# Optimization experiments

Measured on AMD Instinct MI355X. Metric: run time of the kernel, lower is better.

Reference implementation:

```python
import math
import jax, jax.numpy as jnp
import numpy as np

MAX_N = 3; MAX_L = 3
CUTOFF = 5.0; TB_CUTOFF = 4.0; NBLOCKS = 3
N_NODES = 5000; N_EDGES = 60000; N_TRIP = 400000
NELEM = 89; DN = 128; DE = 128; UNITS = 128; DEG = MAX_N * MAX_L

# zeros of spherical bessel j_l, l = 0..2, first 3 roots each
J_ROOTS = np.array([
    [3.141592653589793, 6.283185307179586, 9.42477796076938],
    [4.493409457909064, 7.725251836937707, 10.904121659428899],
    [5.763459196894550, 9.095011330476355, 12.322940970566582],
])

def _jl(l, x, xp):
    s, c = xp.sin(x), xp.cos(x)
    if l == 0:
        return s / x
    if l == 1:
        return s / x**2 - c / x
    if l == 2:
        return (3.0 / x**3 - 1.0 / x) * s - 3.0 * c / x**2
    return (15.0 / x**4 - 6.0 / x**2) * s - (15.0 / x**3 - 1.0 / x) * c

SBF_FACTOR = math.sqrt(2.0 / CUTOFF**3)
SBF_NORM = np.stack([np.abs(_jl(l + 1, J_ROOTS[l], np)) for l in range(MAX_L)])  # [3,3]

def sbf_expand(r):  # [n] -> [n, MAX_L*MAX_N], l-major (matches torch cat over l)
    cols = []
    for l in range(MAX_L):
        x = r[:, None] * (J_ROOTS[l] / CUTOFF)[None, :]
        cols.append(_jl(l, x, jnp) * (SBF_FACTOR / SBF_NORM[l])[None, :])
    return jnp.concatenate(cols, axis=1)

Y00 = 0.28209479177387814  # 0.5*sqrt(1/pi)
Y10 = 0.4886025119029199   # sqrt(3/(4pi))
Y20 = 0.31539156525252005  # 0.25*sqrt(5/pi)

def shf_expand(cos_t):  # [n] -> [n, MAX_L]  real Y_l0(theta)
    return jnp.stack([jnp.full_like(cos_t, Y00), Y10 * cos_t, Y20 * (3.0 * cos_t**2 - 1.0)], axis=1)

def poly_cutoff(r, c):
    x = r / c
    return 1.0 - 6.0 * x**5 + 15.0 * x**4 - 10.0 * x**3

def gated_mlp(x, Ws, bs, gWs, gbs):
    h = x
    for W, b in zip(Ws, bs):
        h = jax.nn.silu(h @ W + b)
    g = x
    n = len(gWs)
    for i, (W, b) in enumerate(zip(gWs, gbs)):
        g = g @ W + b
        g = jax.nn.sigmoid(g) if i == n - 1 else jax.nn.silu(g)
    return h * g

def _forward(pos, node_type, src, dst, t_src, t_dst, emb_table, edge_emb_W, edge_emb_b,
             tb_atom_W, tb_atom_b, tb_bond_W, tb_bond_Wg,
             W0, b0, W1, b1, W2, b2, gW0, gb0, gW1, gb1, gW2, gb2, wt,
             fW0, fb0, fW1, fb1, fW2, fb2):
    n_nodes = pos.shape[0]; n_edges = src.shape[0]
    bond_vec = pos[dst] - pos[src]                              # [E,3]
    bond_dist = jnp.sqrt(jnp.sum(bond_vec**2, axis=1) + 1e-12)  # [E]
    rbf = sbf_expand(bond_dist)                                 # [E,9]
    # triplet (line-graph edge) geometry
    v1, v2 = bond_vec[t_src], bond_vec[t_dst]
    cos_t = jnp.sum(v1 * v2, axis=1) / (bond_dist[t_src] * bond_dist[t_dst])
    three_basis = sbf_expand(bond_dist[t_dst]) * jnp.repeat(shf_expand(cos_t), MAX_N, axis=1)  # [T,9]
    cut3 = poly_cutoff(bond_dist, TB_CUTOFF)
    tw = (cut3[t_src] * cut3[t_dst])[:, None]                   # [T,1]
    end_atom = dst[t_dst]                                       # [T]
    node_feat = emb_table[node_type]                            # [N,DN]
    edge_feat = jax.nn.silu(rbf @ edge_emb_W + edge_emb_b)      # [E,DE]
    for k in range(NBLOCKS):
        # --- three-body interaction ---
        atoms = jax.nn.sigmoid(node_feat @ tb_atom_W[k] + tb_atom_b[k])  # [N,9]
        basis = three_basis * atoms[end_atom] * tw                        # [T,9]
        nb = jax.ops.segment_sum(basis, t_src, num_segments=n_edges)      # [E,9]
        edge_feat = edge_feat + jax.nn.silu(nb @ tb_bond_W[k]) * jax.nn.sigmoid(nb @ tb_bond_Wg[k])
        # --- graph conv: edge update ---
        x = jnp.concatenate([node_feat[src], node_feat[dst], edge_feat], axis=1)  # [E,384]
        e_upd = gated_mlp(x, (W0[k, 0], W1[k, 0], W2[k, 0]), (b0[k, 0], b1[k, 0], b2[k, 0]),
                          (gW0[k, 0], gW1[k, 0], gW2[k, 0]), (gb0[k, 0], gb1[k, 0], gb2[k, 0])) * (rbf @ wt[k, 0])
        edge_feat = edge_feat + e_upd
        # --- graph conv: node update (sum messages at destination) ---
        x = jnp.concatenate([node_feat[src], node_feat[dst], edge_feat], axis=1)
        mess = gated_mlp(x, (W0[k, 1], W1[k, 1], W2[k, 1]), (b0[k, 1], b1[k, 1], b2[k, 1]),
                         (gW0[k, 1], gW1[k, 1], gW2[k, 1]), (gb0[k, 1], gb1[k, 1], gb2[k, 1])) * (rbf @ wt[k, 1])
        node_feat = node_feat + jax.ops.segment_sum(mess, dst, num_segments=n_nodes)
    # ReduceReadOut('mean') over nodes (single graph) + final MLP
    v = jnp.mean(node_feat, axis=0)
    h = jax.nn.silu(v @ fW0 + fb0)
    h = jax.nn.silu(h @ fW1 + fb1)
    return jnp.squeeze(h @ fW2 + fb2)

def setup_inputs() -> dict:
    key = jax.random.key(0)
    ks = iter(jax.random.split(key, 64))
    def nrm(shape, fan_in):
        return jax.random.normal(next(ks), shape, dtype=jnp.float32) / math.sqrt(float(fan_in))
    pos = jax.random.normal(next(ks), (N_NODES, 3), dtype=jnp.float32) * 1.5
    node_type = jax.random.randint(next(ks), (N_NODES,), 0, NELEM, dtype=jnp.int32)
    src = jax.random.randint(next(ks), (N_EDGES,), 0, N_NODES, dtype=jnp.int32)
    dst = (src + 1 + jax.random.randint(next(ks), (N_EDGES,), 0, N_NODES - 1, dtype=jnp.int32)) % N_NODES
    t_src = jax.random.randint(next(ks), (N_TRIP,), 0, N_EDGES, dtype=jnp.int32)
    t_dst = jax.random.randint(next(ks), (N_TRIP,), 0, N_EDGES, dtype=jnp.int32)
    DIN = 2 * DN + DE
    z = lambda *s: jnp.zeros(s, jnp.float32)
    return dict(
        pos=pos, node_type=node_type, src=src, dst=dst, t_src=t_src, t_dst=t_dst,
        emb_table=nrm((NELEM, DN), 1.0),
        edge_emb_W=nrm((DEG, DE), DEG), edge_emb_b=z(DE),
        tb_atom_W=nrm((NBLOCKS, DN, DEG), DN), tb_atom_b=z(NBLOCKS, DEG),
        tb_bond_W=nrm((NBLOCKS, DEG, DE), DEG), tb_bond_Wg=nrm((NBLOCKS, DEG, DE), DEG),
        W0=nrm((NBLOCKS, 2, DIN, UNITS), DIN), b0=z(NBLOCKS, 2, UNITS),
        W1=nrm((NBLOCKS, 2, UNITS, UNITS), UNITS), b1=z(NBLOCKS, 2, UNITS),
        W2=nrm((NBLOCKS, 2, UNITS, DE), UNITS), b2=z(NBLOCKS, 2, DE),
        gW0=nrm((NBLOCKS, 2, DIN, UNITS), DIN), gb0=z(NBLOCKS, 2, UNITS),
        gW1=nrm((NBLOCKS, 2, UNITS, UNITS), UNITS), gb1=z(NBLOCKS, 2, UNITS),
        gW2=nrm((NBLOCKS, 2, UNITS, DE), UNITS), gb2=z(NBLOCKS, 2, DE),
        wt=nrm((NBLOCKS, 2, DEG, DE), DEG),
        fW0=nrm((DN, UNITS), DN), fb0=z(UNITS),
        fW1=nrm((UNITS, UNITS), UNITS), fb1=z(UNITS),
        fW2=nrm((UNITS, 1), UNITS), fb2=z(1))

def reference(pos, node_type, src, dst, t_src, t_dst, emb_table, edge_emb_W, edge_emb_b,
              tb_atom_W, tb_atom_b, tb_bond_W, tb_bond_Wg,
              W0, b0, W1, b1, W2, b2, gW0, gb0, gW1, gb1, gW2, gb2, wt,
              fW0, fb0, fW1, fb1, fW2, fb2):
    return _forward(pos, node_type, src, dst, t_src, t_dst, emb_table, edge_emb_W, edge_emb_b,
                    tb_atom_W, tb_atom_b, tb_bond_W, tb_bond_Wg,
                    W0, b0, W1, b1, W2, b2, gW0, gb0, gW1, gb1, gW2, gb2, wt,
                    fW0, fb0, fW1, fb1, fW2, fb2)
```

## Files before the change

kernel.cpp:

```cpp
#include <hip/hip_runtime.h>
#include <stdint.h>

typedef __attribute__((ext_vector_type(8))) short bf16x8;
typedef __attribute__((ext_vector_type(4))) float f32x4;
typedef __attribute__((ext_vector_type(4))) uint32_t u32x4;

#define XSS 392
#define HSS 144
#define TE 32

__device__ __forceinline__ float sigm(float x) { return __fdividef(1.0f, 1.0f + __expf(-x)); }
__device__ __forceinline__ float silu(float x) { return __fdividef(x, 1.0f + __expf(-x)); }
__device__ __forceinline__ short f2bf(float f) {
  uint32_t u = __float_as_uint(f);
  u = (u + 0x7fffu + ((u >> 16) & 1u)) >> 16;
  return (short)u;
}
__device__ __forceinline__ uint32_t cvt2(float lo, float hi) {
  uint32_t d;
  asm("v_cvt_pk_bf16_f32 %0, %1, %2" : "=v"(d) : "v"(lo), "v"(hi));
  return d;
}
__device__ __forceinline__ short f2bf1(float f) { return (short)cvt2(f, f); }

__device__ __forceinline__ float jl_eval(int l, float x) {
  float s, c;
  sincosf(x, &s, &c);
  float ix = 1.0f / x, ix2 = ix * ix;
  if (l == 0) return s * ix;
  if (l == 1) return s * ix2 - c * ix;
  if (l == 2) return (3.0f * ix2 * ix - ix) * s - 3.0f * ix2 * c;
  return (15.0f * ix2 * ix2 - 6.0f * ix2) * s - (15.0f * ix2 * ix - ix) * c;
}

__global__ void setup1_kernel(const int* __restrict__ ntb, const float* __restrict__ emb,
                              float* __restrict__ nf, int N,
                              const float* __restrict__ pos, const int* __restrict__ src,
                              const int* __restrict__ dst, float* __restrict__ bvec,
                              float* __restrict__ bdist, float* __restrict__ rbf,
                              float* __restrict__ cut3, int E,
                              const int* __restrict__ t_src, int* __restrict__ cnt_e,
                              int* __restrict__ cnt_n, int T) {
  int i = blockIdx.x * 256 + threadIdx.x;
  if (i < N * 128) {
    int n = i >> 7, c = i & 127;
    nf[i] = emb[ntb[n] * 128 + c];
  }
  if (i < E) {
    int s = src[i], d = dst[i];
    float dx = pos[d * 3 + 0] - pos[s * 3 + 0];
    float dy = pos[d * 3 + 1] - pos[s * 3 + 1];
    float dz = pos[d * 3 + 2] - pos[s * 3 + 2];
    float r = sqrtf(dx * dx + dy * dy + dz * dz + 1e-12f);
    bvec[i * 3 + 0] = dx; bvec[i * 3 + 1] = dy; bvec[i * 3 + 2] = dz;
    bdist[i] = r;
    const float roots[3][3] = {
        {3.141592653589793f, 6.283185307179586f, 9.42477796076938f},
        {4.493409457909064f, 7.725251836937707f, 10.904121659428899f},
        {5.763459196894550f, 9.095011330476355f, 12.322940970566582f}};
#pragma unroll
    for (int l = 0; l < 3; ++l) {
#pragma unroll
      for (int n = 0; n < 3; ++n) {
        float root = roots[l][n];
        float x = r * (root * 0.2f);
        float norm = fabsf(jl_eval(l + 1, root));
        rbf[i * 9 + l * 3 + n] = jl_eval(l, x) * (0.12649110640673518f / norm);
      }
    }
    float xx = r * 0.25f;
    float x3 = xx * xx * xx;
    cut3[i] = 1.0f - 6.0f * x3 * xx * xx + 15.0f * x3 * xx - 10.0f * x3;
    atomicAdd(&cnt_n[d], 1);
  }
  if (i < T) atomicAdd(&cnt_e[t_src[i]], 1);
}

__device__ void scan_chunk(const int* __restrict__ in, int* __restrict__ incl,
                           int* __restrict__ bsum, int L, int b) {
  __shared__ int sm[256];
  int i = b * 256 + threadIdx.x;
  int v = i < L ? in[i] : 0;
  sm[threadIdx.x] = v;
  __syncthreads();
  for (int st = 1; st < 256; st <<= 1) {
    int t = threadIdx.x >= st ? sm[threadIdx.x - st] : 0;
    __syncthreads();
    sm[threadIdx.x] += t;
    __syncthreads();
  }
  if (i < L) incl[i] = sm[threadIdx.x];
  if (threadIdx.x == 255) bsum[b] = sm[255];
}

__global__ void setup2_kernel(const float* __restrict__ rbf, const float* __restrict__ eW,
                              const float* __restrict__ eB, float* __restrict__ ef, int E,
                              const int* __restrict__ cnt_e, int* __restrict__ incl_e,
                              int* __restrict__ bsum_e, int ebk,
                              const int* __restrict__ cnt_n, int* __restrict__ incl_n,
                              int* __restrict__ bsum_n, int nbk, int N,
                              const float* __restrict__ nf, const float* __restrict__ taW,
                              const float* __restrict__ taB, float* __restrict__ atoms) {
  int b = blockIdx.x;
  if (b < ebk) scan_chunk(cnt_e, incl_e, bsum_e, E, b);
  else if (b < ebk + nbk) scan_chunk(cnt_n, incl_n, bsum_n, N, b - ebk);
  int i = b * 256 + threadIdx.x;
  if (i < E * 128) {
    int e = i >> 7, c = i & 127;
    float acc = eB[c];
#pragma unroll
    for (int d = 0; d < 9; ++d) acc += rbf[e * 9 + d] * eW[d * 128 + c];
    ef[i] = silu(acc);
  }
  if (i < N * 9) {
    int n = i / 9, d = i - n * 9;
    float acc = taB[d];
    for (int c = 0; c < 128; ++c) acc += nf[n * 128 + c] * taW[c * 9 + d];
    atoms[i] = sigm(acc);
  }
}

__global__ void scan_top2_kernel(int* __restrict__ bsum_e, int ne, int* __restrict__ bsum_n,
                                 int nn) {
  __shared__ int sm[1024];
  int* bs = blockIdx.x == 0 ? bsum_e : bsum_n;
  int nb = blockIdx.x == 0 ? ne : nn;
  int tid = threadIdx.x;
  int orig = tid < nb ? bs[tid] : 0;
  sm[tid] = orig;
  __syncthreads();
  for (int st = 1; st < 1024; st <<= 1) {
    int t = tid >= st ? sm[tid - st] : 0;
    __syncthreads();
    sm[tid] += t;
    __syncthreads();
  }
  if (tid < nb) bs[tid] = sm[tid] - orig;
}

__global__ void fin2_kernel(const int* __restrict__ cnt_e, const int* __restrict__ incl_e,
                            const int* __restrict__ bsum_e, int ebk, int* __restrict__ off_e,
                            int* __restrict__ cur_e, int E, const int* __restrict__ cnt_n,
                            const int* __restrict__ incl_n, const int* __restrict__ bsum_n,
                            int* __restrict__ off_n, int* __restrict__ cur_n, int N) {
  int b = blockIdx.x;
  if (b < ebk) {
    int i = b * 256 + threadIdx.x;
    if (i < E) {
      int o = incl_e[i] - cnt_e[i] + bsum_e[b];
      off_e[i] = o; cur_e[i] = o;
    }
  } else {
    int bb = b - ebk;
    int i = bb * 256 + threadIdx.x;
    if (i < N) {
      int o = incl_n[i] - cnt_n[i] + bsum_n[bb];
      off_n[i] = o; cur_n[i] = o;
    }
  }
}

__global__ void build_kernel(const int* __restrict__ t_src, const int* __restrict__ t_dst,
                             const int* __restrict__ dst, const float* __restrict__ bvec,
                             const float* __restrict__ bdist, const float* __restrict__ rbf,
                             const float* __restrict__ cut3, int* __restrict__ cur_e,
                             float* __restrict__ stbp, int* __restrict__ sa, int T,
                             int* __restrict__ cur_n, int* __restrict__ invp, int E) {
  int t = blockIdx.x * 256 + threadIdx.x;
  if (t < T) {
    int i = t_src[t], j = t_dst[t];
    float ax = bvec[i * 3], ay = bvec[i * 3 + 1], az = bvec[i * 3 + 2];
    float bx = bvec[j * 3], by = bvec[j * 3 + 1], bz = bvec[j * 3 + 2];
    float ct = (ax * bx + ay * by + az * bz) / (bdist[i] * bdist[j]);
    float tw = cut3[i] * cut3[j];
    float sh[3];
    sh[0] = 0.28209479177387814f * tw;
    sh[1] = 0.4886025119029199f * ct * tw;
    sh[2] = 0.31539156525252005f * (3.0f * ct * ct - 1.0f) * tw;
    int pos = atomicAdd(&cur_e[i], 1);
#pragma unroll
    for (int l = 0; l < 3; ++l)
#pragma unroll
      for (int n = 0; n < 3; ++n)
        stbp[(size_t)pos * 9 + l * 3 + n] = rbf[j * 9 + l * 3 + n] * sh[l];
    sa[pos] = dst[j];
  }
  if (t < E) {
    int pos = atomicAdd(&cur_n[dst[t]], 1);
    invp[t] = pos;
  }
}

__device__ void pack_one(const float* __restrict__ Wf, short* __restrict__ Wp, int K, int rr) {
  int per = 8 * (K / 32) * 64;
  int u = rr / per, r2 = rr - u * per;
  int lane = r2 & 63, tile = r2 >> 6;
  int kt = tile % (K / 32), nt = tile / (K / 32);
  int n = nt * 16 + (lane & 15);
  int k0 = kt * 32 + (lane >> 4) * 8;
  const float* s = Wf + (size_t)u * K * 128;
  bf16x8 v;
#pragma unroll
  for (int e = 0; e < 8; ++e) v[e] = f2bf(s[(size_t)(k0 + e) * 128 + n]);
  *(bf16x8*)(Wp + (size_t)u * K * 128 + (size_t)tile * 512 + lane * 8) = v;
}

__device__ void pack_pad9(const float* __restrict__ s, short* __restrict__ dp9, int l2) {
  int lane = l2 & 63, tile = l2 >> 6;
  int n = tile * 16 + (lane & 15);
  int k0 = (lane >> 4) * 8;
  bf16x8 v;
#pragma unroll
  for (int e = 0; e < 8; ++e)
    v[e] = (k0 + e < 9) ? f2bf(s[(size_t)(k0 + e) * 128 + n]) : (short)0;
  *(bf16x8*)(dp9 + tile * 512 + lane * 8) = v;
}

__global__ void pack_all_kernel(const float* __restrict__ W0, const float* __restrict__ G0,
                                const float* __restrict__ W1, const float* __restrict__ G1,
                                const float* __restrict__ W2, const float* __restrict__ G2,
                                const float* __restrict__ tbW, const float* __restrict__ tbG,
                                const float* __restrict__ WT,
                                short* __restrict__ pW0, short* __restrict__ pG0,
                                short* __restrict__ pW1, short* __restrict__ pG1,
                                short* __restrict__ pW2, short* __restrict__ pG2,
                                short* __restrict__ ptbW, short* __restrict__ ptbG,
                                short* __restrict__ pWT) {
  int idx = blockIdx.x * 256 + threadIdx.x;
  const int t384 = 6 * 8 * 12 * 64, t128 = 6 * 8 * 4 * 64;
  if (idx < t384) { pack_one(W0, pW0, 384, idx); return; }
  if (idx < 2 * t384) { pack_one(G0, pG0, 384, idx - t384); return; }
  int j = idx - 2 * t384;
  if (j < t128) { pack_one(W1, pW1, 128, j); return; }
  if (j < 2 * t128) { pack_one(G1, pG1, 128, j - t128); return; }
  if (j < 3 * t128) { pack_one(W2, pW2, 128, j - 2 * t128); return; }
  if (j < 4 * t128) { pack_one(G2, pG2, 128, j - 3 * t128); return; }
  j -= 4 * t128;
  if (j < 3072) {
    int kb = j >> 10;
    int w2 = (j >> 9) & 1;
    int l2 = j & 511;
    const float* s = (w2 ? tbG : tbW) + (size_t)kb * 9 * 128;
    short* dp = (w2 ? ptbG : ptbW) + (size_t)kb * 4096;
    pack_pad9(s, dp, l2);
    return;
  }
  j -= 3072;
  if (j < 3072) {
    int u = j >> 9;
    pack_pad9(WT + (size_t)u * 9 * 128, pWT + (size_t)u * 4096, j & 511);
  }
}

__device__ __forceinline__ f32x4 mfma16(bf16x8 a, bf16x8 b, f32x4 c) {
  return __builtin_amdgcn_mfma_f32_16x16x32_bf16(a, b, c, 0, 0, 0);
}

__device__ __forceinline__ void store_hg(short* hsb, short* gsb, int wave, int lane,
                                         const f32x4 (&aW)[2], const f32x4 (&aG)[2]) {
  const int lrow = lane & 15, lk = lane >> 4;
  const int colx = (wave * 16 + lrow) ^ (lk << 4);
#pragma unroll
  for (int mt = 0; mt < 2; ++mt)
#pragma unroll
    for (int rg = 0; rg < 4; ++rg) {
      int row = mt * 16 + lk * 4 + rg;
      hsb[row * HSS + colx] = f2bf1(silu(aW[mt][rg]));
      gsb[row * HSS + colx] = f2bf1(silu(aG[mt][rg]));
    }
}

__device__ __forceinline__ void layer128w(const short* hin, const short* gin,
                                          const short* __restrict__ pW,
                                          const short* __restrict__ pG,
                                          const float* __restrict__ Bh,
                                          const float* __restrict__ Bg, int wave, int lane,
                                          f32x4 (&aW)[2], f32x4 (&aG)[2]) {
  const int lrow = lane & 15, lk = lane >> 4;
  const int s0 = (lrow >> 2) & 3;
  float bw = Bh[wave * 16 + lrow], bg = Bg[wave * 16 + lrow];
  aW[0] = {bw, bw, bw, bw}; aW[1] = aW[0];
  aG[0] = {bg, bg, bg, bg}; aG[1] = aG[0];
#pragma unroll
  for (int kt = 0; kt < 4; ++kt) {
    int aoff = (kt * 32 + lk * 8) ^ (s0 << 4);
    bf16x8 ah0 = *(const bf16x8*)(hin + (size_t)lrow * HSS + aoff);
    bf16x8 ah1 = *(const bf16x8*)(hin + (size_t)(16 + lrow) * HSS + aoff);
    bf16x8 ag0 = *(const bf16x8*)(gin + (size_t)lrow * HSS + aoff);
    bf16x8 ag1 = *(const bf16x8*)(gin + (size_t)(16 + lrow) * HSS + aoff);
    bf16x8 bw8 = *(const bf16x8*)(pW + (size_t)(wave * 4 + kt) * 512 + lane * 8);
    bf16x8 bg8 = *(const bf16x8*)(pG + (size_t)(wave * 4 + kt) * 512 + lane * 8);
    aW[0] = mfma16(ah0, bw8, aW[0]);
    aW[1] = mfma16(ah1, bw8, aW[1]);
    aG[0] = mfma16(ag0, bg8, aG[0]);
    aG[1] = mfma16(ag1, bg8, aG[1]);
  }
}

__device__ __forceinline__ void run_chain(
    const short* xsb, short* hsb, short* gsb,
    const short* __restrict__ pW0, const short* __restrict__ pG0,
    const short* __restrict__ pW1, const short* __restrict__ pG1,
    const short* __restrict__ pW2, const short* __restrict__ pG2,
    const float* __restrict__ B0, const float* __restrict__ Gb0,
    const float* __restrict__ B1, const float* __restrict__ Gb1,
    const float* __restrict__ B2, const float* __restrict__ Gb2,
    int wave, int lane, f32x4 (&aW)[2], f32x4 (&aG)[2]) {
  const int lrow = lane & 15, lk = lane >> 4;
  const int s0 = (lrow >> 2) & 3;
  {
    float bw = B0[wave * 16 + lrow], bg = Gb0[wave * 16 + lrow];
    aW[0] = {bw, bw, bw, bw}; aW[1] = aW[0];
    aG[0] = {bg, bg, bg, bg}; aG[1] = aG[0];
  }
#pragma unroll
  for (int kt = 0; kt < 12; ++kt) {
    int al = kt * 32 + lk * 8;
    int aoff = (al < 256) ? al : (256 + ((al - 256) ^ (s0 << 4)));
    bf16x8 a0 = *(const bf16x8*)(xsb + (size_t)lrow * XSS + aoff);
    bf16x8 a1 = *(const bf16x8*)(xsb + (size_t)(16 + lrow) * XSS + aoff);
    bf16x8 bw8 = *(const bf16x8*)(pW0 + (size_t)(wave * 12 + kt) * 512 + lane * 8);
    bf16x8 bg8 = *(const bf16x8*)(pG0 + (size_t)(wave * 12 + kt) * 512 + lane * 8);
    aW[0] = mfma16(a0, bw8, aW[0]);
    aW[1] = mfma16(a1, bw8, aW[1]);
    aG[0] = mfma16(a0, bg8, aG[0]);
    aG[1] = mfma16(a1, bg8, aG[1]);
  }
  store_hg(hsb, gsb, wave, lane, aW, aG);
  __syncthreads();
  layer128w(hsb, gsb, pW1, pG1, B1, Gb1, wave, lane, aW, aG);
  __syncthreads();
  store_hg(hsb, gsb, wave, lane, aW, aG);
  __syncthreads();
  layer128w(hsb, gsb, pW2, pG2, B2, Gb2, wave, lane, aW, aG);
}

__global__ __launch_bounds__(512, 6) void gmlp_fused(
    const float* __restrict__ nf, float* __restrict__ ef, const float* __restrict__ rbf,
    const int* __restrict__ src, const int* __restrict__ dst,
    const float* __restrict__ stbp, const int* __restrict__ sa,
    const int* __restrict__ off_e, const int* __restrict__ cnt_e,
    const float* __restrict__ atoms, const int* __restrict__ invp,
    const short* __restrict__ ptbW, const short* __restrict__ ptbG,
    const short* __restrict__ pW0a, const short* __restrict__ pG0a,
    const short* __restrict__ pW1a, const short* __restrict__ pG1a,
    const short* __restrict__ pW2a, const short* __restrict__ pG2a,
    const float* __restrict__ B0a, const float* __restrict__ Gb0a,
    const float* __restrict__ B1a, const float* __restrict__ Gb1a,
    const float* __restrict__ B2a, const float* __restrict__ Gb2a,
    const short* __restrict__ pWTa,
    const short* __restrict__ pW0b, const short* __restrict__ pG0b,
    const short* __restrict__ pW1b, const short* __restrict__ pG1b,
    const short* __restrict__ pW2b, const short* __restrict__ pG2b,
    const float* __restrict__ B0b, const float* __restrict__ Gb0b,
    const float* __restrict__ B1b, const float* __restrict__ Gb1b,
    const float* __restrict__ B2b, const float* __restrict__ Gb2b,
    const short* __restrict__ pWTb,
    float* __restrict__ mbuf, int E, int writeEf) {
  __shared__ __align__(16) short xs[32][XSS];
  __shared__ __align__(16) short hs[32 * HSS];
  __shared__ __align__(16) short gs[32 * HSS];
  __shared__ __align__(16) short nbl[32][40];
  __shared__ __align__(16) short rbl[32][40];
  __shared__ int invs[32];
  const int tid = threadIdx.x;
  const int e0 = blockIdx.x * TE;
  const int r = tid >> 4, q = tid & 15;
  int eg = e0 + r; if (eg >= E) eg = E - 1;

  {
    float acc = 0.f;
    if (q < 9) {
      int o = off_e[eg], c = cnt_e[eg];
      for (int pp = o; pp < o + c; ++pp)
        acc += stbp[(size_t)pp * 9 + q] * atoms[(size_t)sa[pp] * 9 + q];
    }
    nbl[r][q] = (q < 9) ? f2bf1(acc) : (short)0;
    nbl[r][q + 16] = 0;
  }
  {
    const float* sp0 = nf + (size_t)src[eg] * 128;
    const float* sp1 = nf + (size_t)dst[eg] * 128;
#pragma unroll
    for (int seg = 0; seg < 2; ++seg) {
      const float* sp = seg == 0 ? sp0 : sp1;
      float4 f0 = *(const float4*)(sp + q * 8);
      float4 f1 = *(const float4*)(sp + q * 8 + 4);
      u32x4 v = {cvt2(f0.x, f0.y), cvt2(f0.z, f0.w), cvt2(f1.x, f1.y), cvt2(f1.z, f1.w)};
      *(u32x4*)&xs[r][seg * 128 + q * 8] = v;
    }
    for (int idx = tid; idx < 32 * 32; idx += 512) {
      int rr = idx >> 5, d = idx & 31;
      int ee = e0 + rr; if (ee >= E) ee = E - 1;
      rbl[rr][d] = (d < 9) ? f2bf1(rbf[ee * 9 + d]) : (short)0;
    }
    if (tid < 32) {
      int ee = e0 + tid; if (ee >= E) ee = E - 1;
      invs[tid] = invp[ee];
    }
  }
  __syncthreads();

  const int wave = tid >> 6;
  const int lane = tid & 63;
  const int lrow = lane & 15, lk = lane >> 4;
  const int col = wave * 16 + lrow;
  f32x4 aW[2], aG[2];
  float efb[2][4];

  {
    bf16x8 ta0 = *(const bf16x8*)&nbl[lrow][lk * 8];
    bf16x8 ta1 = *(const bf16x8*)&nbl[16 + lrow][lk * 8];
    bf16x8 tbw = *(const bf16x8*)(ptbW + wave * 512 + lane * 8);
    bf16x8 tbg = *(const bf16x8*)(ptbG + wave * 512 + lane * 8);
    f32x4 z = {0.f, 0.f, 0.f, 0.f};
    f32x4 tW0 = mfma16(ta0, tbw, z), tW1 = mfma16(ta1, tbw, z);
    f32x4 tG0 = mfma16(ta0, tbg, z), tG1 = mfma16(ta1, tbg, z);
#pragma unroll
    for (int mt = 0; mt < 2; ++mt)
#pragma unroll
      for (int rg = 0; rg < 4; ++rg) {
        int row = mt * 16 + lk * 4 + rg;
        int ec = e0 + row; if (ec >= E) ec = E - 1;
        float tw = mt == 0 ? tW0[rg] : tW1[rg];
        float tg = mt == 0 ? tG0[rg] : tG1[rg];
        float base = ef[(size_t)ec * 128 + col] + silu(tw) * sigm(tg);
        efb[mt][rg] = base;
        xs[row][256 + (col ^ (lk << 4))] = f2bf1(base);
      }
  }
  __syncthreads();

  run_chain(&xs[0][0], hs, gs, pW0a, pG0a, pW1a, pG1a, pW2a, pG2a,
            B0a, Gb0a, B1a, Gb1a, B2a, Gb2a, wave, lane, aW, aG);
  {
    bf16x8 ra0 = *(const bf16x8*)&rbl[lrow][lk * 8];
    bf16x8 ra1 = *(const bf16x8*)&rbl[16 + lrow][lk * 8];
    bf16x8 wtb = *(const bf16x8*)(pWTa + wave * 512 + lane * 8);
    f32x4 z = {0.f, 0.f, 0.f, 0.f};
    f32x4 wv0 = mfma16(ra0, wtb, z), wv1 = mfma16(ra1, wtb, z);
    const int cs = 256 + (col ^ (lk << 4));
#pragma unroll
    for (int mt = 0; mt < 2; ++mt)
#pragma unroll
      for (int rg = 0; rg < 4; ++rg) {
        int row = mt * 16 + lk * 4 + rg;
        int e = e0 + row;
        float wv = mt == 0 ? wv0[rg] : wv1[rg];
        float v = silu(aW[mt][rg]) * sigm(aG[mt][rg]) * wv;
        float nv = efb[mt][rg] + v;
        if (e < E && writeEf) ef[(size_t)e * 128 + col] = nv;
        xs[row][cs] = f2bf1(nv);
      }
  }
  __syncthreads();

  run_chain(&xs[0][0], hs, gs, pW0b, pG0b, pW1b, pG1b, pW2b, pG2b,
            B0b, Gb0b, B1b, Gb1b, B2b, Gb2b, wave, lane, aW, aG);
  {
    bf16x8 ra0 = *(const bf16x8*)&rbl[lrow][lk * 8];
    bf16x8 ra1 = *(const bf16x8*)&rbl[16 + lrow][lk * 8];
    bf16x8 wtb = *(const bf16x8*)(pWTb + wave * 512 + lane * 8);
    f32x4 z = {0.f, 0.f, 0.f, 0.f};
    f32x4 wv0 = mfma16(ra0, wtb, z), wv1 = mfma16(ra1, wtb, z);
#pragma unroll
    for (int mt = 0; mt < 2; ++mt)
#pragma unroll
      for (int rg = 0; rg < 4; ++rg) {
        int row = mt * 16 + lk * 4 + rg;
        int e = e0 + row;
        float wv = mt == 0 ? wv0[rg] : wv1[rg];
        float v = silu(aW[mt][rg]) * sigm(aG[mt][rg]) * wv;
        if (e < E) mbuf[(size_t)invs[row] * 128 + col] = v;
      }
  }
}

__global__ void node_gather_kernel(float* __restrict__ nf, const float* __restrict__ mbuf,
                                   const int* __restrict__ off_n, const int* __restrict__ cnt_n,
                                   const float* __restrict__ taW, const float* __restrict__ taB,
                                   float* __restrict__ atoms, int N, int doAtoms) {
  __shared__ float sm[2][128];
  int half = threadIdx.x >> 7, c = threadIdx.x & 127;
  int n = blockIdx.x * 2 + half;
  float v = 0.f;
  if (n < N) {
    int o = off_n[n], cnt = cnt_n[n];
    float acc = 0.f;
    for (int p = 0; p < cnt; ++p) acc += mbuf[(size_t)(o + p) * 128 + c];
    v = nf[(size_t)n * 128 + c] + acc;
    nf[(size_t)n * 128 + c] = v;
  }
  if (doAtoms) {
    sm[half][c] = v;
    __syncthreads();
    if (n < N && c < 9) {
      float a = taB[c];
      for (int cc = 0; cc < 128; ++cc) a += sm[half][cc] * taW[cc * 9 + c];
      atoms[n * 9 + c] = sigm(a);
    }
  }
}

__global__ void mean_kernel(const float* __restrict__ nf, float* __restrict__ partial, int N) {
  __shared__ float sm[256];
  int n0 = blockIdx.x * 256;
  int col = threadIdx.x & 127, half = threadIdx.x >> 7;
  int nend = n0 + 256 < N ? n0 + 256 : N;
  float s = 0.f;
  for (int n = n0 + half; n < nend; n += 2) s += nf[n * 128 + col];
  sm[threadIdx.x] = s;
  __syncthreads();
  if (threadIdx.x < 128)
    partial[blockIdx.x * 128 + threadIdx.x] = sm[threadIdx.x] + sm[threadIdx.x + 128];
}

__global__ void final_kernel(const float* __restrict__ partial, int nchunks, float Nf,
                             const float* __restrict__ fW0, const float* __restrict__ fb0,
                             const float* __restrict__ fW1, const float* __restrict__ fb1,
                             const float* __restrict__ fW2, const float* __restrict__ fb2,
                             float* __restrict__ out) {
  __shared__ float v[128], h[128], red[128];
  int tid = threadIdx.x;
  float s = 0.f;
  for (int b = 0; b < nchunks; ++b) s += partial[b * 128 + tid];
  v[tid] = s / Nf;
  __syncthreads();
  float acc = fb0[tid];
  for (int c = 0; c < 128; ++c) acc += v[c] * fW0[c * 128 + tid];
  h[tid] = silu(acc);
  __syncthreads();
  acc = fb1[tid];
  for (int c = 0; c < 128; ++c) acc += h[c] * fW1[c * 128 + tid];
  __syncthreads();
  v[tid] = silu(acc);
  __syncthreads();
  red[tid] = v[tid] * fW2[tid];
  __syncthreads();
  for (int st = 64; st > 0; st >>= 1) {
    if (tid < st) red[tid] += red[tid + st];
    __syncthreads();
  }
  if (tid == 0) out[0] = red[0] + fb2[0];
}

extern "C" void kernel_launch(void* const* d_in, const int* in_sizes, int n_in,
                              void* d_out, int out_size, void* d_ws, size_t ws_size,
                              hipStream_t stream) {
  const float* pos = (const float*)d_in[0];
  const int* node_type = (const int*)d_in[1];
  const int* src = (const int*)d_in[2];
  const int* dst = (const int*)d_in[3];
  const int* t_src = (const int*)d_in[4];
  const int* t_dst = (const int*)d_in[5];
  const float* emb = (const float*)d_in[6];
  const float* eW = (const float*)d_in[7];
  const float* eB = (const float*)d_in[8];
  const float* taW = (const float*)d_in[9];
  const float* taB = (const float*)d_in[10];
  const float* tbW = (const float*)d_in[11];
  const float* tbG = (const float*)d_in[12];
  const float* W0 = (const float*)d_in[13]; const float* B0 = (const float*)d_in[14];
  const float* W1 = (const float*)d_in[15]; const float* B1 = (const float*)d_in[16];
  const float* W2 = (const float*)d_in[17]; const float* B2 = (const float*)d_in[18];
  const float* G0 = (const float*)d_in[19]; const float* Gb0 = (const float*)d_in[20];
  const float* G1 = (const float*)d_in[21]; const float* Gb1 = (const float*)d_in[22];
  const float* G2 = (const float*)d_in[23]; const float* Gb2 = (const float*)d_in[24];
  const float* WT = (const float*)d_in[25];
  const float* fW0 = (const float*)d_in[26]; const float* fb0 = (const float*)d_in[27];
  const float* fW1 = (const float*)d_in[28]; const float* fb1 = (const float*)d_in[29];
  const float* fW2 = (const float*)d_in[30]; const float* fb2 = (const float*)d_in[31];

  const int N = in_sizes[1];
  const int E = in_sizes[2];
  const int T = in_sizes[4];

  char* p = (char*)d_ws;
  auto alloc = [&](size_t bytes) -> char* {
    char* r = p;
    p += (bytes + 255) & ~(size_t)255;
    return r;
  };
  float* nf    = (float*)alloc((size_t)N * 128 * 4);
  float* ef    = (float*)alloc((size_t)E * 128 * 4);
  float* mbuf  = (float*)alloc((size_t)E * 128 * 4);
  float* rbf   = (float*)alloc((size_t)E * 9 * 4);
  float* bvec  = (float*)alloc((size_t)E * 3 * 4);
  float* bdist = (float*)alloc((size_t)E * 4);
  float* cut3  = (float*)alloc((size_t)E * 4);
  float* stbp  = (float*)alloc((size_t)T * 9 * 4);
  int*   sa    = (int*)alloc((size_t)T * 4);
  float* atoms = (float*)alloc((size_t)N * 9 * 4);
  float* part  = (float*)alloc((size_t)64 * 128 * 4);
  int* cnt_all = (int*)alloc((size_t)(E + N) * 4);
  int* cnt_e = cnt_all, *cnt_n = cnt_all + E;
  int* incl_e = (int*)alloc((size_t)E * 4);
  int* incl_n = (int*)alloc((size_t)N * 4);
  int* off_e  = (int*)alloc((size_t)E * 4);
  int* off_n  = (int*)alloc((size_t)N * 4);
  int* cur_e  = (int*)alloc((size_t)E * 4);
  int* cur_n  = (int*)alloc((size_t)N * 4);
  int* invp   = (int*)alloc((size_t)E * 4);
  int* bsum_e = (int*)alloc((size_t)1024 * 4);
  int* bsum_n = (int*)alloc((size_t)1024 * 4);
  short* pW0s = (short*)alloc((size_t)6 * 384 * 128 * 2);
  short* pG0s = (short*)alloc((size_t)6 * 384 * 128 * 2);
  short* pW1s = (short*)alloc((size_t)6 * 128 * 128 * 2);
  short* pG1s = (short*)alloc((size_t)6 * 128 * 128 * 2);
  short* pW2s = (short*)alloc((size_t)6 * 128 * 128 * 2);
  short* pG2s = (short*)alloc((size_t)6 * 128 * 128 * 2);
  short* ptbWs = (short*)alloc((size_t)3 * 4096 * 2);
  short* ptbGs = (short*)alloc((size_t)3 * 4096 * 2);
  short* pWTs  = (short*)alloc((size_t)6 * 4096 * 2);
  (void)ws_size; (void)n_in; (void)out_size;

  const int ebk = (E + 255) / 256, nbk = (N + 255) / 256;

  pack_all_kernel<<<504, 256, 0, stream>>>(W0, G0, W1, G1, W2, G2, tbW, tbG, WT,
                                           pW0s, pG0s, pW1s, pG1s, pW2s, pG2s,
                                           ptbWs, ptbGs, pWTs);
  hipMemsetAsync(cnt_all, 0, (size_t)(E + N) * 4, stream);
  {
    int g1 = N * 128; if (E > g1) g1 = E; if (T > g1) g1 = T;
    setup1_kernel<<<(g1 + 255) / 256, 256, 0, stream>>>(
        node_type, emb, nf, N, pos, src, dst, bvec, bdist, rbf, cut3, E, t_src, cnt_e, cnt_n, T);
  }
  {
    int g2 = E * 128; int g2b = (ebk + nbk) * 256; if (g2b > g2) g2 = g2b;
    if (N * 9 > g2) g2 = N * 9;
    setup2_kernel<<<(g2 + 255) / 256, 256, 0, stream>>>(
        rbf, eW, eB, ef, E, cnt_e, incl_e, bsum_e, ebk, cnt_n, incl_n, bsum_n, nbk, N,
        nf, taW, taB, atoms);
  }
  scan_top2_kernel<<<2, 1024, 0, stream>>>(bsum_e, ebk, bsum_n, nbk);
  fin2_kernel<<<ebk + nbk, 256, 0, stream>>>(cnt_e, incl_e, bsum_e, ebk, off_e, cur_e, E,
                                             cnt_n, incl_n, bsum_n, off_n, cur_n, N);
  {
    int g3 = T > E ? T : E;
    build_kernel<<<(g3 + 255) / 256, 256, 0, stream>>>(t_src, t_dst, dst, bvec, bdist, rbf,
                                                       cut3, cur_e, stbp, sa, T, cur_n, invp, E);
  }

  const int gblocks = (E + TE - 1) / TE;
  for (int k = 0; k < 3; ++k) {
    size_t u0 = (size_t)(k * 2 + 0), u1 = u0 + 1;
    gmlp_fused<<<gblocks, 512, 0, stream>>>(
        nf, ef, rbf, src, dst, stbp, sa, off_e, cnt_e, atoms, invp,
        ptbWs + (size_t)k * 4096, ptbGs + (size_t)k * 4096,
        pW0s + u0 * 384 * 128, pG0s + u0 * 384 * 128, pW1s + u0 * 128 * 128,
        pG1s + u0 * 128 * 128, pW2s + u0 * 128 * 128, pG2s + u0 * 128 * 128,
        B0 + u0 * 128, Gb0 + u0 * 128, B1 + u0 * 128, Gb1 + u0 * 128, B2 + u0 * 128,
        Gb2 + u0 * 128, pWTs + u0 * 4096,
        pW0s + u1 * 384 * 128, pG0s + u1 * 384 * 128, pW1s + u1 * 128 * 128,
        pG1s + u1 * 128 * 128, pW2s + u1 * 128 * 128, pG2s + u1 * 128 * 128,
        B0 + u1 * 128, Gb0 + u1 * 128, B1 + u1 * 128, Gb1 + u1 * 128, B2 + u1 * 128,
        Gb2 + u1 * 128, pWTs + u1 * 4096,
        mbuf, E, k < 2 ? 1 : 0);
    int nk = k < 2 ? k + 1 : 0;
    node_gather_kernel<<<(N + 1) / 2, 256, 0, stream>>>(
        nf, mbuf, off_n, cnt_n, taW + (size_t)nk * 128 * 9, taB + (size_t)nk * 9,
        atoms, N, k < 2 ? 1 : 0);
  }

  int nchunks = (N + 255) / 256;
  mean_kernel<<<nchunks, 256, 0, stream>>>(nf, part, N);
  final_kernel<<<1, 128, 0, stream>>>(part, nchunks, (float)N, fW0, fb0, fW1, fb1, fW2, fb2,
                                      (float*)d_out);
}
```

Baseline: 516.3 us.

## Store edge features, messages and triplet bases in bf16 and hoist weight MFMAs

Edge features, per-edge messages and the three-body basis buffers move from fp32 to bf16 storage, roughly halving their global memory traffic in the fused edge kernel and the node gather. The edge feature row is now loaded as one vector into the shared tile during prologue staging, replacing scattered scalar global reads. Both rbf-weight MFMAs are hoisted to the start of the kernel. This keeps the residual edge state in bf16 between blocks, which costs accuracy, and the hoisted results raise register pressure.

```diff
diff --git a/kernel.cpp b/kernel.cpp
--- a/kernel.cpp
+++ b/kernel.cpp
@@ -4,6 +4,7 @@
 typedef __attribute__((ext_vector_type(8))) short bf16x8;
 typedef __attribute__((ext_vector_type(4))) float f32x4;
 typedef __attribute__((ext_vector_type(4))) uint32_t u32x4;
+typedef unsigned short ushort;
 
 #define XSS 392
 #define HSS 144
@@ -16,6 +17,7 @@
   u = (u + 0x7fffu + ((u >> 16) & 1u)) >> 16;
   return (short)u;
 }
+__device__ __forceinline__ float bf2f(ushort u) { return __uint_as_float(((uint32_t)u) << 16); }
 __device__ __forceinline__ uint32_t cvt2(float lo, float hi) {
   uint32_t d;
   asm("v_cvt_pk_bf16_f32 %0, %1, %2" : "=v"(d) : "v"(lo), "v"(hi));
@@ -94,7 +96,7 @@
 }
 
 __global__ void setup2_kernel(const float* __restrict__ rbf, const float* __restrict__ eW,
-                              const float* __restrict__ eB, float* __restrict__ ef, int E,
+                              const float* __restrict__ eB, ushort* __restrict__ ef, int E,
                               const int* __restrict__ cnt_e, int* __restrict__ incl_e,
                               int* __restrict__ bsum_e, int ebk,
                               const int* __restrict__ cnt_n, int* __restrict__ incl_n,
@@ -110,7 +112,7 @@
     float acc = eB[c];
 #pragma unroll
     for (int d = 0; d < 9; ++d) acc += rbf[e * 9 + d] * eW[d * 128 + c];
-    ef[i] = silu(acc);
+    ef[i] = (ushort)f2bf1(silu(acc));
   }
   if (i < N * 9) {
     int n = i / 9, d = i - n * 9;
@@ -164,7 +166,7 @@
                              const int* __restrict__ dst, const float* __restrict__ bvec,
                              const float* __restrict__ bdist, const float* __restrict__ rbf,
                              const float* __restrict__ cut3, int* __restrict__ cur_e,
-                             float* __restrict__ stbp, int* __restrict__ sa, int T,
+                             ushort* __restrict__ stbp, int* __restrict__ sa, int T,
                              int* __restrict__ cur_n, int* __restrict__ invp, int E) {
   int t = blockIdx.x * 256 + threadIdx.x;
   if (t < T) {
@@ -182,7 +184,7 @@
     for (int l = 0; l < 3; ++l)
 #pragma unroll
       for (int n = 0; n < 3; ++n)
-        stbp[(size_t)pos * 9 + l * 3 + n] = rbf[j * 9 + l * 3 + n] * sh[l];
+        stbp[(size_t)pos * 9 + l * 3 + n] = (ushort)f2bf(rbf[j * 9 + l * 3 + n] * sh[l]);
     sa[pos] = dst[j];
   }
   if (t < E) {
@@ -336,9 +338,9 @@
 }
 
 __global__ __launch_bounds__(512, 6) void gmlp_fused(
-    const float* __restrict__ nf, float* __restrict__ ef, const float* __restrict__ rbf,
+    const float* __restrict__ nf, ushort* __restrict__ ef, const float* __restrict__ rbf,
     const int* __restrict__ src, const int* __restrict__ dst,
-    const float* __restrict__ stbp, const int* __restrict__ sa,
+    const ushort* __restrict__ stbp, const int* __restrict__ sa,
     const int* __restrict__ off_e, const int* __restrict__ cnt_e,
     const float* __restrict__ atoms, const int* __restrict__ invp,
     const short* __restrict__ ptbW, const short* __restrict__ ptbG,
@@ -356,7 +358,7 @@
     const float* __restrict__ B1b, const float* __restrict__ Gb1b,
     const float* __restrict__ B2b, const float* __restrict__ Gb2b,
     const short* __restrict__ pWTb,
-    float* __restrict__ mbuf, int E, int writeEf) {
+    ushort* __restrict__ mbuf, int E, int writeEf) {
   __shared__ __align__(16) short xs[32][XSS];
   __shared__ __align__(16) short hs[32 * HSS];
   __shared__ __align__(16) short gs[32 * HSS];
@@ -366,6 +368,7 @@
   const int tid = threadIdx.x;
   const int e0 = blockIdx.x * TE;
   const int r = tid >> 4, q = tid & 15;
+  const int sr = (r >> 2) & 3;
   int eg = e0 + r; if (eg >= E) eg = E - 1;
 
   {
@@ -373,7 +376,7 @@
     if (q < 9) {
       int o = off_e[eg], c = cnt_e[eg];
       for (int pp = o; pp < o + c; ++pp)
-        acc += stbp[(size_t)pp * 9 + q] * atoms[(size_t)sa[pp] * 9 + q];
+        acc += bf2f(stbp[(size_t)pp * 9 + q]) * atoms[(size_t)sa[pp] * 9 + q];
     }
     nbl[r][q] = (q < 9) ? f2bf1(acc) : (short)0;
     nbl[r][q + 16] = 0;
@@ -389,6 +392,8 @@
       u32x4 v = {cvt2(f0.x, f0.y), cvt2(f0.z, f0.w), cvt2(f1.x, f1.y), cvt2(f1.z, f1.w)};
       *(u32x4*)&xs[r][seg * 128 + q * 8] = v;
     }
+    bf16x8 ev = *(const bf16x8*)(ef + (size_t)eg * 128 + q * 8);
+    *(bf16x8*)&xs[r][256 + ((q * 8) ^ (sr << 4))] = ev;
     for (int idx = tid; idx < 32 * 32; idx += 512) {
       int rr = idx >> 5, d = idx & 31;
       int ee = e0 + rr; if (ee >= E) ee = E - 1;
@@ -405,28 +410,35 @@
   const int lane = tid & 63;
   const int lrow = lane & 15, lk = lane >> 4;
   const int col = wave * 16 + lrow;
+  const int cs = 256 + (col ^ (lk << 4));
   f32x4 aW[2], aG[2];
   float efb[2][4];
+  f32x4 wva0, wva1, wvb0, wvb1;
 
   {
     bf16x8 ta0 = *(const bf16x8*)&nbl[lrow][lk * 8];
     bf16x8 ta1 = *(const bf16x8*)&nbl[16 + lrow][lk * 8];
     bf16x8 tbw = *(const bf16x8*)(ptbW + wave * 512 + lane * 8);
     bf16x8 tbg = *(const bf16x8*)(ptbG + wave * 512 + lane * 8);
+    bf16x8 ra0 = *(const bf16x8*)&rbl[lrow][lk * 8];
+    bf16x8 ra1 = *(const bf16x8*)&rbl[16 + lrow][lk * 8];
+    bf16x8 wta = *(const bf16x8*)(pWTa + wave * 512 + lane * 8);
+    bf16x8 wtb = *(const bf16x8*)(pWTb + wave * 512 + lane * 8);
     f32x4 z = {0.f, 0.f, 0.f, 0.f};
     f32x4 tW0 = mfma16(ta0, tbw, z), tW1 = mfma16(ta1, tbw, z);
     f32x4 tG0 = mfma16(ta0, tbg, z), tG1 = mfma16(ta1, tbg, z);
+    wva0 = mfma16(ra0, wta, z); wva1 = mfma16(ra1, wta, z);
+    wvb0 = mfma16(ra0, wtb, z); wvb1 = mfma16(ra1, wtb, z);
 #pragma unroll
     for (int mt = 0; mt < 2; ++mt)
 #pragma unroll
       for (int rg = 0; rg < 4; ++rg) {
         int row = mt * 16 + lk * 4 + rg;
-        int ec = e0 + row; if (ec >= E) ec = E - 1;
         float tw = mt == 0 ? tW0[rg] : tW1[rg];
         float tg = mt == 0 ? tG0[rg] : tG1[rg];
-        float base = ef[(size_t)ec * 128 + col] + silu(tw) * sigm(tg);
+        float base = bf2f((ushort)xs[row][cs]) + silu(tw) * sigm(tg);
         efb[mt][rg] = base;
-        xs[row][256 + (col ^ (lk << 4))] = f2bf1(base);
+        xs[row][cs] = f2bf1(base);
       }
   }
   __syncthreads();
@@ -434,23 +446,18 @@
   run_chain(&xs[0][0], hs, gs, pW0a, pG0a, pW1a, pG1a, pW2a, pG2a,
             B0a, Gb0a, B1a, Gb1a, B2a, Gb2a, wave, lane, aW, aG);
   {
-    bf16x8 ra0 = *(const bf16x8*)&rbl[lrow][lk * 8];
-    bf16x8 ra1 = *(const bf16x8*)&rbl[16 + lrow][lk * 8];
-    bf16x8 wtb = *(const bf16x8*)(pWTa + wave * 512 + lane * 8);
-    f32x4 z = {0.f, 0.f, 0.f, 0.f};
-    f32x4 wv0 = mfma16(ra0, wtb, z), wv1 = mfma16(ra1, wtb, z);
-    const int cs = 256 + (col ^ (lk << 4));
 #pragma unroll
     for (int mt = 0; mt < 2; ++mt)
 #pragma unroll
       for (int rg = 0; rg < 4; ++rg) {
         int row = mt * 16 + lk * 4 + rg;
         int e = e0 + row;
-        float wv = mt == 0 ? wv0[rg] : wv1[rg];
+        float wv = mt == 0 ? wva0[rg] : wva1[rg];
         float v = silu(aW[mt][rg]) * sigm(aG[mt][rg]) * wv;
         float nv = efb[mt][rg] + v;
-        if (e < E && writeEf) ef[(size_t)e * 128 + col] = nv;
-        xs[row][cs] = f2bf1(nv);
+        short sv = f2bf1(nv);
+        if (e < E && writeEf) ef[(size_t)e * 128 + col] = (ushort)sv;
+        xs[row][cs] = sv;
       }
   }
   __syncthreads();
@@ -458,25 +465,20 @@
   run_chain(&xs[0][0], hs, gs, pW0b, pG0b, pW1b, pG1b, pW2b, pG2b,
             B0b, Gb0b, B1b, Gb1b, B2b, Gb2b, wave, lane, aW, aG);
   {
-    bf16x8 ra0 = *(const bf16x8*)&rbl[lrow][lk * 8];
-    bf16x8 ra1 = *(const bf16x8*)&rbl[16 + lrow][lk * 8];
-    bf16x8 wtb = *(const bf16x8*)(pWTb + wave * 512 + lane * 8);
-    f32x4 z = {0.f, 0.f, 0.f, 0.f};
-    f32x4 wv0 = mfma16(ra0, wtb, z), wv1 = mfma16(ra1, wtb, z);
 #pragma unroll
     for (int mt = 0; mt < 2; ++mt)
 #pragma unroll
       for (int rg = 0; rg < 4; ++rg) {
         int row = mt * 16 + lk * 4 + rg;
         int e = e0 + row;
-        float wv = mt == 0 ? wv0[rg] : wv1[rg];
+        float wv = mt == 0 ? wvb0[rg] : wvb1[rg];
         float v = silu(aW[mt][rg]) * sigm(aG[mt][rg]) * wv;
-        if (e < E) mbuf[(size_t)invs[row] * 128 + col] = v;
+        if (e < E) mbuf[(size_t)invs[row] * 128 + col] = (ushort)f2bf1(v);
       }
   }
 }
 
-__global__ void node_gather_kernel(float* __restrict__ nf, const float* __restrict__ mbuf,
+__global__ void node_gather_kernel(float* __restrict__ nf, const ushort* __restrict__ mbuf,
                                    const int* __restrict__ off_n, const int* __restrict__ cnt_n,
                                    const float* __restrict__ taW, const float* __restrict__ taB,
                                    float* __restrict__ atoms, int N, int doAtoms) {
@@ -487,7 +489,7 @@
   if (n < N) {
     int o = off_n[n], cnt = cnt_n[n];
     float acc = 0.f;
-    for (int p = 0; p < cnt; ++p) acc += mbuf[(size_t)(o + p) * 128 + c];
+    for (int p = 0; p < cnt; ++p) acc += bf2f(mbuf[(size_t)(o + p) * 128 + c]);
     v = nf[(size_t)n * 128 + c] + acc;
     nf[(size_t)n * 128 + c] = v;
   }
@@ -581,17 +583,17 @@
     p += (bytes + 255) & ~(size_t)255;
     return r;
   };
-  float* nf    = (float*)alloc((size_t)N * 128 * 4);
-  float* ef    = (float*)alloc((size_t)E * 128 * 4);
-  float* mbuf  = (float*)alloc((size_t)E * 128 * 4);
-  float* rbf   = (float*)alloc((size_t)E * 9 * 4);
-  float* bvec  = (float*)alloc((size_t)E * 3 * 4);
-  float* bdist = (float*)alloc((size_t)E * 4);
-  float* cut3  = (float*)alloc((size_t)E * 4);
-  float* stbp  = (float*)alloc((size_t)T * 9 * 4);
-  int*   sa    = (int*)alloc((size_t)T * 4);
-  float* atoms = (float*)alloc((size_t)N * 9 * 4);
-  float* part  = (float*)alloc((size_t)64 * 128 * 4);
+  float*  nf    = (float*)alloc((size_t)N * 128 * 4);
+  ushort* ef    = (ushort*)alloc((size_t)E * 128 * 2);
+  ushort* mbuf  = (ushort*)alloc((size_t)E * 128 * 2);
+  float*  rbf   = (float*)alloc((size_t)E * 9 * 4);
+  float*  bvec  = (float*)alloc((size_t)E * 3 * 4);
+  float*  bdist = (float*)alloc((size_t)E * 4);
+  float*  cut3  = (float*)alloc((size_t)E * 4);
+  ushort* stbp  = (ushort*)alloc((size_t)T * 9 * 2);
+  int*    sa    = (int*)alloc((size_t)T * 4);
+  float*  atoms = (float*)alloc((size_t)N * 9 * 4);
+  float*  part  = (float*)alloc((size_t)64 * 128 * 4);
   int* cnt_all = (int*)alloc((size_t)(E + N) * 4);
   int* cnt_e = cnt_all, *cnt_n = cnt_all + E;
   int* incl_e = (int*)alloc((size_t)E * 4);
```

Measured after the change: 537.7 us. 1.04x slower.
